# Performance work log

Measured on AMD Instinct MI355X. Metric: run time of the kernel, lower is better.

The kernel has to match this reference:

```python
import jax, jax.numpy as jnp
import numpy as np

HEADS = 12
DIM_HEAD = 64
SCALE = DIM_HEAD ** -0.5


def rotate_every_two(x):
    # (..., 2d) -> rotate pairs: (x1, x2) -> (-x2, x1)
    x = x.reshape(*x.shape[:-1], -1, 2)
    x1, x2 = x[..., 0], x[..., 1]
    return jnp.stack((-x2, x1), axis=-1).reshape(*x.shape[:-2], -1)


def apply_rotary_pos_emb(q, k, sinu_pos):
    # sinu_pos: (b, p, 2c) -> sin, cos each (b, p, c)
    b, p, two_c = sinu_pos.shape
    sp = sinu_pos.reshape(b, p, 2, two_c // 2)
    sin, cos = sp[:, :, 0, :], sp[:, :, 1, :]
    # interleave-repeat to (b, 1, p, 2c) to broadcast over heads
    sin = jnp.repeat(sin, 2, axis=-1)[:, None, :, :]
    cos = jnp.repeat(cos, 2, axis=-1)[:, None, :, :]
    rot = lambda t: t * cos + rotate_every_two(t) * sin
    return rot(q), rot(k)


def setup_inputs() -> dict:
    key = jax.random.key(0)
    ks = jax.random.split(key, 5)
    b, n, dim = 8, 1024, 768
    inner = HEADS * DIM_HEAD
    x = jax.random.normal(ks[0], (b, n, dim), dtype=jnp.float32)
    pos_emb = jax.random.normal(ks[1], (1, n, DIM_HEAD), dtype=jnp.float32)
    W_qkv = jax.random.normal(ks[2], (dim, 3 * inner), dtype=jnp.float32) * (dim ** -0.5)
    W_out = jax.random.normal(ks[3], (inner, dim), dtype=jnp.float32) * (inner ** -0.5)
    b_out = jnp.zeros((dim,), dtype=jnp.float32)
    return {"x": x, "pos_emb": pos_emb, "W_qkv": W_qkv, "W_out": W_out, "b_out": b_out}


def reference(x, pos_emb, W_qkv, W_out, b_out):
    b, n, _ = x.shape
    qkv = x @ W_qkv                                   # (b, n, 3*inner)
    q, k, v = jnp.split(qkv, 3, axis=-1)
    split_heads = lambda t: t.reshape(b, n, HEADS, DIM_HEAD).transpose(0, 2, 1, 3)
    q, k, v = split_heads(q), split_heads(k), split_heads(v)   # (b, h, n, d)
    q, k = apply_rotary_pos_emb(q, k, pos_emb)
    dots = jnp.einsum('bhid,bhjd->bhij', q, k) * SCALE
    attn = jax.nn.softmax(dots, axis=-1)
    out = jnp.einsum('bhij,bhjd->bhid', attn, v)
    out = out.transpose(0, 2, 1, 3).reshape(b, n, HEADS * DIM_HEAD)
    out = out @ W_out + b_out
    return out  # context is None -> torch code returns (out[:, :n], None); n == full length
```

## Files before the change

kernel.cpp:

```cpp
#include <hip/hip_runtime.h>
#include <hip/hip_bf16.h>

typedef __attribute__((ext_vector_type(8))) short bf16x8;
typedef __attribute__((ext_vector_type(4))) float f32x4;
typedef __attribute__((ext_vector_type(4))) unsigned short u16x4;
typedef unsigned short u16;
typedef unsigned int u32;

#define DEVINL __device__ __forceinline__

DEVINL u16 f2bf(float f) {
    union { float f; u32 u; } v; v.f = f;
    u32 r = v.u + 0x7FFFu + ((v.u >> 16) & 1u);
    return (u16)(r >> 16);
}
DEVINL float bf2f(u16 h) {
    union { u32 u; float f; } v; v.u = ((u32)h) << 16;
    return v.f;
}
DEVINL u32 cvt_pk_bf16(float lo, float hi) {
    u32 r;
    asm("v_cvt_pk_bf16_f32 %0, %1, %2" : "=v"(r) : "v"(lo), "v"(hi));
    return r;
}

template<int Nv> DEVINL void vmcnt_asm() {
    if constexpr (Nv == 0) asm volatile("s_waitcnt vmcnt(0)" ::: "memory");
    else if constexpr (Nv == 3) asm volatile("s_waitcnt vmcnt(3)" ::: "memory");
    else if constexpr (Nv == 5) asm volatile("s_waitcnt vmcnt(5)" ::: "memory");
    else if constexpr (Nv == 6) asm volatile("s_waitcnt vmcnt(6)" ::: "memory");
    else if constexpr (Nv == 7) asm volatile("s_waitcnt vmcnt(7)" ::: "memory");
    else asm volatile("s_waitcnt vmcnt(4)" ::: "memory");
}

#define GLOAD_LDS16(g, l) __builtin_amdgcn_global_load_lds( \
    (const __attribute__((address_space(1))) void*)(g), \
    (__attribute__((address_space(3))) void*)(l), 16, 0, 0)

#define SBAR() do { \
    __builtin_amdgcn_sched_barrier(0); \
    __builtin_amdgcn_s_barrier(); \
    __builtin_amdgcn_sched_barrier(0); } while (0)

__global__ __launch_bounds__(256) void prep_kernel(const float* __restrict__ x,
                                                   u16* __restrict__ xb,
                                                   const float* __restrict__ W_qkv,
                                                   u16* __restrict__ Wqkv_t,
                                                   const float* __restrict__ W_out,
                                                   u16* __restrict__ Wout_t) {
    __shared__ float tile[32][33];
    const int bid = blockIdx.x;
    if (bid < 3072) {
        int t = bid * 256 + threadIdx.x;
        const float4 v0 = reinterpret_cast<const float4*>(x)[t * 2];
        const float4 v1 = reinterpret_cast<const float4*>(x)[t * 2 + 1];
        u16 o[8];
        o[0] = f2bf(v0.x); o[1] = f2bf(v0.y); o[2] = f2bf(v0.z); o[3] = f2bf(v0.w);
        o[4] = f2bf(v1.x); o[5] = f2bf(v1.y); o[6] = f2bf(v1.z); o[7] = f2bf(v1.w);
        *reinterpret_cast<bf16x8*>(xb + (size_t)t * 8) = *reinterpret_cast<bf16x8*>(o);
        return;
    }
    const float* in; u16* out; int R, C, bx, by;
    if (bid < 4800) {
        int u = bid - 3072; in = W_qkv; out = Wqkv_t; R = 768; C = 2304;
        bx = u % 72; by = u / 72;
    } else {
        int u = bid - 4800; in = W_out; out = Wout_t; R = 768; C = 768;
        bx = u % 24; by = u / 24;
    }
    int c0 = bx * 32, r0 = by * 32;
    int tx = threadIdx.x & 31, ty = threadIdx.x >> 5;
#pragma unroll
    for (int i = 0; i < 4; ++i)
        tile[ty + i * 8][tx] = in[(size_t)(r0 + ty + i * 8) * C + c0 + tx];
    __syncthreads();
#pragma unroll
    for (int i = 0; i < 4; ++i)
        out[(size_t)(c0 + ty + i * 8) * R + r0 + tx] = f2bf(tile[tx][ty + i * 8]);
}

template<int K>
__global__ __launch_bounds__(256, 3) void gemm1_kernel(const u16* __restrict__ A,
                                                       const u16* __restrict__ Bt,
                                                       u16* __restrict__ Cout) {
    constexpr int NT = K / 32;
    constexpr int PBUF = (128 + 192) * 32;
    __shared__ u16 lds[2 * PBUF];

    const int tid = threadIdx.x;
    const int wv = tid >> 6, lane = tid & 63;
    const int lr = lane & 15, lg = lane >> 4;
    const int wr = wv >> 1, wc = wv & 1;

    const int id = blockIdx.x;
    const int sid = (id & 7) * 96 + (id >> 3);
    const int bm = (sid / 12) * 128;
    const int bn = (sid % 12) * 192;

#define STAGE(nb_, kt_) do { \
    _Pragma("unroll") \
    for (int j_ = 0; j_ < 2; ++j_) { \
        const int idx_ = j_ * 256 + tid; \
        const int row_ = idx_ >> 2; \
        const int c_ = (idx_ & 3) ^ ((row_ >> 1) & 3); \
        GLOAD_LDS16(A + (size_t)(bm + row_) * K + (kt_) * 32 + c_ * 8, \
                    (char*)lds + (nb_) * (PBUF * 2) + j_ * 4096 + tid * 16); \
    } \
    _Pragma("unroll") \
    for (int j_ = 0; j_ < 3; ++j_) { \
        const int idx_ = j_ * 256 + tid; \
        const int row_ = idx_ >> 2; \
        const int c_ = (idx_ & 3) ^ ((row_ >> 1) & 3); \
        GLOAD_LDS16(Bt + (size_t)(bn + row_) * K + (kt_) * 32 + c_ * 8, \
                    (char*)lds + (nb_) * (PBUF * 2) + 8192 + j_ * 4096 + tid * 16); \
    } } while (0)

    f32x4 acc[4][6];
#pragma unroll
    for (int i = 0; i < 4; ++i)
#pragma unroll
        for (int j = 0; j < 6; ++j) acc[i][j] = (f32x4){0.f, 0.f, 0.f, 0.f};

    STAGE(0, 0);
    __builtin_amdgcn_sched_barrier(0);
    vmcnt_asm<0>();
    SBAR();

    for (int kt = 0; kt < NT; ++kt) {
        const int cur = kt & 1;
        if (kt < NT - 1) {
            STAGE(cur ^ 1, kt + 1);
            __builtin_amdgcn_sched_barrier(0);
            vmcnt_asm<5>();
            SBAR();
        } else {
            __builtin_amdgcn_sched_barrier(0);
            vmcnt_asm<0>();
            SBAR();
        }
        bf16x8 af[4], bfr[6];
#pragma unroll
        for (int mf = 0; mf < 4; ++mf) {
            const int row = wr * 64 + mf * 16 + lr;
            af[mf] = *reinterpret_cast<const bf16x8*>(
                &lds[cur * PBUF + row * 32 + ((lg ^ ((row >> 1) & 3)) << 3)]);
        }
#pragma unroll
        for (int nf = 0; nf < 6; ++nf) {
            const int row = wc * 96 + nf * 16 + lr;
            bfr[nf] = *reinterpret_cast<const bf16x8*>(
                &lds[cur * PBUF + 4096 + row * 32 + ((lg ^ ((row >> 1) & 3)) << 3)]);
        }
        __builtin_amdgcn_s_setprio(1);
#pragma unroll
        for (int mf = 0; mf < 4; ++mf)
#pragma unroll
            for (int nf = 0; nf < 6; ++nf)
                acc[mf][nf] = __builtin_amdgcn_mfma_f32_16x16x32_bf16(
                    af[mf], bfr[nf], acc[mf][nf], 0, 0, 0);
        __builtin_amdgcn_s_setprio(0);
        SBAR();
    }

#pragma unroll
    for (int mf = 0; mf < 4; ++mf)
#pragma unroll
        for (int nf = 0; nf < 6; ++nf) {
            const int col = bn + wc * 96 + nf * 16 + lr;
#pragma unroll
            for (int r = 0; r < 4; ++r) {
                const int row = bm + wr * 64 + mf * 16 + lg * 4 + r;
                Cout[(size_t)row * 2304 + col] = f2bf(acc[mf][nf][r]);
            }
        }
#undef STAGE
}

template<int NTN, int NFRAG, int BROWS, int K, bool BF16_OUT>
__global__ __launch_bounds__(512, 2) void gemm_bigtile_kernel(const u16* __restrict__ A,
                                                              const u16* __restrict__ Bt,
                                                              void* __restrict__ Cout,
                                                              const float* __restrict__ bias) {
    constexpr int BN = NFRAG * 32;
    constexpr int N = NTN * BN;
    constexpr int NT = K / 64;
    constexpr int PA = 256 * 32;
    constexpr int PB = BROWS * 32;
    constexpr int PKS = PA + PB;
    constexpr int PBUF = 2 * PKS;
    constexpr int BFULL = (BROWS * 4) / 512;
    constexpr int BREM = (BROWS * 4) % 512;
    __shared__ u16 lds[2 * PBUF];

    const int tid = threadIdx.x;
    const int wv = tid >> 6, lane = tid & 63;
    const int lr = lane & 15, lg = lane >> 4;
    const int wr = wv >> 1, wc = wv & 1;

    const int id = blockIdx.x;
    const int sid = (id & 7) * 32 + (id >> 3);
    const int bm = (sid / NTN) * 256;
    const int bn = (sid % NTN) * BN;

#define PL(buf_, ks_, mat_) ((buf_) * PBUF + (ks_) * PKS + (mat_) * PA)

#define STAGE_A(nb_, kt_, ks_) do { \
    _Pragma("unroll") \
    for (int j_ = 0; j_ < 2; ++j_) { \
        const int idx_ = j_ * 512 + tid; \
        const int row_ = idx_ >> 2; \
        const int c_ = (idx_ & 3) ^ ((row_ >> 1) & 3); \
        GLOAD_LDS16(A + (size_t)(bm + row_) * K + (kt_) * 64 + (ks_) * 32 + c_ * 8, \
                    (char*)lds + PL((nb_), (ks_), 0) * 2 + j_ * 8192 + tid * 16); \
    } } while (0)

#define STAGE_B(nb_, kt_, ks_) do { \
    _Pragma("unroll") \
    for (int j_ = 0; j_ < BFULL; ++j_) { \
        const int idx_ = j_ * 512 + tid; \
        const int row_ = idx_ >> 2; \
        const int c_ = (idx_ & 3) ^ ((row_ >> 1) & 3); \
        GLOAD_LDS16(Bt + (size_t)(bn + row_) * K + (kt_) * 64 + (ks_) * 32 + c_ * 8, \
                    (char*)lds + PL((nb_), (ks_), 1) * 2 + j_ * 8192 + tid * 16); \
    } \
    if constexpr (BREM != 0) { \
        if (tid < BREM) { \
            const int idx_ = BFULL * 512 + tid; \
            const int row_ = idx_ >> 2; \
            const int c_ = (idx_ & 3) ^ ((row_ >> 1) & 3); \
            GLOAD_LDS16(Bt + (size_t)(bn + row_) * K + (kt_) * 64 + (ks_) * 32 + c_ * 8, \
                        (char*)lds + PL((nb_), (ks_), 1) * 2 + BFULL * 8192 + tid * 16); \
        } \
    } } while (0)

#define LDA(mh_, ks_, cur_) do { \
    _Pragma("unroll") \
    for (int f_ = 0; f_ < 2; ++f_) { \
        const int row_ = wr * 64 + (mh_) * 32 + f_ * 16 + lr; \
        af[f_] = *reinterpret_cast<const bf16x8*>( \
            &lds[PL((cur_), (ks_), 0) + row_ * 32 + ((lg ^ ((row_ >> 1) & 3)) << 3)]); \
    } } while (0)

#define LDB(ks_, cur_) do { \
    _Pragma("unroll") \
    for (int nf_ = 0; nf_ < NFRAG; ++nf_) { \
        const int row_ = wc * (NFRAG * 16) + nf_ * 16 + lr; \
        bfr[nf_] = *reinterpret_cast<const bf16x8*>( \
            &lds[PL((cur_), (ks_), 1) + row_ * 32 + ((lg ^ ((row_ >> 1) & 3)) << 3)]); \
    } } while (0)

#define MFMAQ(mh_) do { \
    __builtin_amdgcn_s_setprio(1); \
    _Pragma("unroll") \
    for (int f_ = 0; f_ < 2; ++f_) \
    _Pragma("unroll") \
    for (int nf_ = 0; nf_ < NFRAG; ++nf_) \
        acc[(mh_) * 2 + f_][nf_] = __builtin_amdgcn_mfma_f32_16x16x32_bf16( \
            af[f_], bfr[nf_], acc[(mh_) * 2 + f_][nf_], 0, 0, 0); \
    __builtin_amdgcn_s_setprio(0); } while (0)

#define WAITHALF() do { \
    __builtin_amdgcn_sched_barrier(0); \
    if constexpr (BREM != 0) { \
        if (wv < BREM / 64) vmcnt_asm<2 + BFULL + 1>(); \
        else vmcnt_asm<2 + BFULL>(); \
    } else { \
        vmcnt_asm<2 + BFULL>(); \
    } } while (0)

    f32x4 acc[4][NFRAG];
#pragma unroll
    for (int i = 0; i < 4; ++i)
#pragma unroll
        for (int j = 0; j < NFRAG; ++j) acc[i][j] = (f32x4){0.f, 0.f, 0.f, 0.f};

    bf16x8 af[2], bfr[NFRAG];

    STAGE_A(0, 0, 0); STAGE_B(0, 0, 0); STAGE_A(0, 0, 1); STAGE_B(0, 0, 1);
    __builtin_amdgcn_sched_barrier(0);
    vmcnt_asm<0>();
    SBAR();

    for (int kt = 0; kt < NT - 1; ++kt) {
        const int cur = kt & 1, nxt = cur ^ 1;
        LDB(0, cur); LDA(0, 0, cur);
        STAGE_A(nxt, kt + 1, 0);
        SBAR(); MFMAQ(0); SBAR();
        LDA(1, 0, cur);
        STAGE_B(nxt, kt + 1, 0);
        WAITHALF();
        SBAR(); MFMAQ(1); SBAR();
        LDB(1, cur); LDA(0, 1, cur);
        STAGE_A(nxt, kt + 1, 1);
        SBAR(); MFMAQ(0); SBAR();
        LDA(1, 1, cur);
        STAGE_B(nxt, kt + 1, 1);
        WAITHALF();
        SBAR(); MFMAQ(1); SBAR();
    }
    {
        const int cur = (NT - 1) & 1;
        LDB(0, cur); LDA(0, 0, cur); SBAR(); MFMAQ(0); SBAR();
        LDA(1, 0, cur);
        __builtin_amdgcn_sched_barrier(0);
        vmcnt_asm<0>();
        SBAR(); MFMAQ(1); SBAR();
        LDB(1, cur); LDA(0, 1, cur); SBAR(); MFMAQ(0); SBAR();
        LDA(1, 1, cur); SBAR(); MFMAQ(1);
    }

#pragma unroll
    for (int mf = 0; mf < 4; ++mf)
#pragma unroll
        for (int nf = 0; nf < NFRAG; ++nf) {
            const int col = bn + wc * (NFRAG * 16) + nf * 16 + lr;
            const float bv = BF16_OUT ? 0.f : bias[col];
#pragma unroll
            for (int r = 0; r < 4; ++r) {
                const int row = bm + wr * 64 + mf * 16 + lg * 4 + r;
                if (BF16_OUT)
                    ((u16*)Cout)[(size_t)row * N + col] = f2bf(acc[mf][nf][r]);
                else
                    ((float*)Cout)[(size_t)row * N + col] = acc[mf][nf][r] + bv;
            }
        }
#undef PL
#undef STAGE_A
#undef STAGE_B
#undef LDA
#undef LDB
#undef MFMAQ
#undef WAITHALF
}

__global__ __launch_bounds__(256) void rot_vtrans_kernel(u16* __restrict__ qkv,
                                                         const float* __restrict__ pos,
                                                         u16* __restrict__ Vt) {
    __shared__ u16 tile[64][72];
    const int bid = blockIdx.x;
    if (bid < 6144) {
        int t = bid * 256 + threadIdx.x;
        int row = t / 192;
        int col = (t % 192) * 8;
        int n = row & 1023;
        int i0 = (col & 63) >> 1;
        const float qs = (col < 768) ? 0.18033688f : 1.0f;
        const float* pn = pos + (size_t)n * 64;
        u16* p = qkv + (size_t)row * 2304 + col;
        bf16x8 v = *reinterpret_cast<bf16x8*>(p);
        u16 o[8];
#pragma unroll
        for (int j = 0; j < 4; ++j) {
            float s = pn[i0 + j], c = pn[32 + i0 + j];
            float x0 = bf2f((u16)v[2 * j]), x1 = bf2f((u16)v[2 * j + 1]);
            o[2 * j]     = f2bf((x0 * c - x1 * s) * qs);
            o[2 * j + 1] = f2bf((x1 * c + x0 * s) * qs);
        }
        *reinterpret_cast<bf16x8*>(p) = *reinterpret_cast<bf16x8*>(o);
    } else {
        int u = bid - 6144;
        int nt = u & 15;
        int bh = u >> 4;
        int b = bh / 12, h = bh % 12;
        int tid = threadIdx.x;
        int rr = tid >> 3, cc = (tid & 7) * 8;
#pragma unroll
        for (int it = 0; it < 2; ++it) {
            int nloc = it * 32 + rr;
            const u16* src = qkv + (size_t)(b * 1024 + nt * 64 + nloc) * 2304 + 1536 + h * 64 + cc;
            bf16x8 v = *reinterpret_cast<const bf16x8*>(src);
#pragma unroll
            for (int j = 0; j < 8; ++j) tile[nloc][cc + j] = (u16)v[j];
        }
        __syncthreads();
#pragma unroll
        for (int it = 0; it < 2; ++it) {
            int d = it * 32 + rr;
            u16 o[8];
#pragma unroll
            for (int j = 0; j < 8; ++j) o[j] = tile[cc + j][d];
            *reinterpret_cast<bf16x8*>(Vt + (size_t)(bh * 64 + d) * 1024 + nt * 64 + cc) =
                *reinterpret_cast<bf16x8*>(o);
        }
    }
}

__global__ __launch_bounds__(256, 3) void attn_kernel(const u16* __restrict__ qkv,
                                                      const u16* __restrict__ Vt,
                                                      u16* __restrict__ attn_out) {
    __shared__ u16 Ks[2][64 * 64];
    __shared__ u16 Vs[2][64 * 64];
    const int d_ = blockIdx.x;
    const int bh = ((d_ >> 3) >> 3) * 8 + (d_ & 7);
    const int qt = (d_ >> 3) & 7;
    const int b = bh / 12, h = bh % 12;
    const int tid = threadIdx.x;
    const int w = tid >> 6, lr = tid & 15, lg = (tid >> 4) & 3;

    bf16x8 qf[2][2];
#pragma unroll
    for (int q = 0; q < 2; ++q)
#pragma unroll
        for (int ds = 0; ds < 2; ++ds)
            qf[q][ds] = *reinterpret_cast<const bf16x8*>(
                &qkv[(size_t)(b * 1024 + qt * 128 + w * 32 + q * 16 + lr) * 2304 +
                     h * 64 + ds * 32 + lg * 8]);

    f32x4 o[2][4];
#pragma unroll
    for (int q = 0; q < 2; ++q)
#pragma unroll
        for (int i = 0; i < 4; ++i) o[q][i] = (f32x4){0.f, 0.f, 0.f, 0.f};
    float lsum[2] = {0.f, 0.f};

#define STAGE_KV(nb, kt_) do { \
    _Pragma("unroll") \
    for (int j_ = 0; j_ < 2; ++j_) { \
        const int idx_ = j_ * 256 + tid; \
        const int row_ = idx_ >> 3; \
        const int sc_ = ((idx_ & 7) ^ (row_ & 7)) * 8; \
        const int rk_ = (row_ & 0x20) | ((row_ & 0x0C) << 1) | ((row_ & 0x10) >> 2) | (row_ & 3); \
        GLOAD_LDS16(qkv + (size_t)(b * 1024 + (kt_) * 64 + rk_) * 2304 + 768 + h * 64 + sc_, \
                    (char*)Ks[nb] + idx_ * 16); \
        GLOAD_LDS16(Vt + (size_t)(bh * 64 + row_) * 1024 + (kt_) * 64 + sc_, \
                    (char*)Vs[nb] + idx_ * 16); \
    } } while (0)

    STAGE_KV(0, 0);
    __syncthreads();

    const int rsw = lr & 7;

    for (int kt = 0; kt < 16; ++kt) {
        const int cur = kt & 1;
        if (kt < 15) STAGE_KV(cur ^ 1, kt + 1);

        f32x4 s[2][4];
        __builtin_amdgcn_s_setprio(1);
#pragma unroll
        for (int kf = 0; kf < 4; ++kf) {
            bf16x8 k0 = *reinterpret_cast<const bf16x8*>(
                &Ks[cur][(kf * 16 + lr) * 64 + ((lg ^ rsw) * 8)]);
            bf16x8 k1 = *reinterpret_cast<const bf16x8*>(
                &Ks[cur][(kf * 16 + lr) * 64 + (((4 + lg) ^ rsw) * 8)]);
#pragma unroll
            for (int q = 0; q < 2; ++q) {
                f32x4 a = __builtin_amdgcn_mfma_f32_16x16x32_bf16(
                    k0, qf[q][0], (f32x4){0.f, 0.f, 0.f, 0.f}, 0, 0, 0);
                s[q][kf] = __builtin_amdgcn_mfma_f32_16x16x32_bf16(k1, qf[q][1], a, 0, 0, 0);
            }
        }
        __builtin_amdgcn_s_setprio(0);

        union { u32 wd[4]; bf16x8 v; } pk[2][2];
#pragma unroll
        for (int q = 0; q < 2; ++q) {
#pragma unroll
            for (int kf = 0; kf < 4; ++kf)
#pragma unroll
                for (int r = 0; r < 4; ++r) s[q][kf][r] = __builtin_amdgcn_exp2f(s[q][kf][r]);
            float t0 = (s[q][0][0] + s[q][0][1]) + (s[q][0][2] + s[q][0][3]);
            float t1 = (s[q][1][0] + s[q][1][1]) + (s[q][1][2] + s[q][1][3]);
            float t2 = (s[q][2][0] + s[q][2][1]) + (s[q][2][2] + s[q][2][3]);
            float t3 = (s[q][3][0] + s[q][3][1]) + (s[q][3][2] + s[q][3][3]);
            lsum[q] += (t0 + t1) + (t2 + t3);
#pragma unroll
            for (int ks = 0; ks < 2; ++ks) {
                pk[q][ks].wd[0] = cvt_pk_bf16(s[q][2 * ks][0], s[q][2 * ks][1]);
                pk[q][ks].wd[1] = cvt_pk_bf16(s[q][2 * ks][2], s[q][2 * ks][3]);
                pk[q][ks].wd[2] = cvt_pk_bf16(s[q][2 * ks + 1][0], s[q][2 * ks + 1][1]);
                pk[q][ks].wd[3] = cvt_pk_bf16(s[q][2 * ks + 1][2], s[q][2 * ks + 1][3]);
            }
        }

        __builtin_amdgcn_s_setprio(1);
#pragma unroll
        for (int ks = 0; ks < 2; ++ks) {
#pragma unroll
            for (int df = 0; df < 4; ++df) {
                bf16x8 vb = *reinterpret_cast<const bf16x8*>(
                    &Vs[cur][(df * 16 + lr) * 64 + (((ks * 4 + lg) ^ rsw) * 8)]);
                o[0][df] = __builtin_amdgcn_mfma_f32_16x16x32_bf16(vb, pk[0][ks].v, o[0][df], 0, 0, 0);
                o[1][df] = __builtin_amdgcn_mfma_f32_16x16x32_bf16(vb, pk[1][ks].v, o[1][df], 0, 0, 0);
            }
        }
        __builtin_amdgcn_s_setprio(0);
        __syncthreads();
    }
#undef STAGE_KV

#pragma unroll
    for (int q = 0; q < 2; ++q) {
        float l = lsum[q];
        l += __shfl_xor(l, 16);
        l += __shfl_xor(l, 32);
        const float linv = 1.0f / l;
        u16* orow = attn_out +
            (size_t)(b * 1024 + qt * 128 + w * 32 + q * 16 + lr) * 768 + h * 64 + lg * 4;
#pragma unroll
        for (int df = 0; df < 4; ++df) {
            uint2 st;
            st.x = cvt_pk_bf16(o[q][df][0] * linv, o[q][df][1] * linv);
            st.y = cvt_pk_bf16(o[q][df][2] * linv, o[q][df][3] * linv);
            *reinterpret_cast<uint2*>(orow + df * 16) = st;
        }
    }
}

extern "C" void kernel_launch(void* const* d_in, const int* in_sizes, int n_in,
                              void* d_out, int out_size, void* d_ws, size_t ws_size,
                              hipStream_t stream) {
    (void)in_sizes; (void)n_in; (void)out_size; (void)ws_size;
    const float* x     = (const float*)d_in[0];
    const float* pos   = (const float*)d_in[1];
    const float* W_qkv = (const float*)d_in[2];
    const float* W_out = (const float*)d_in[3];
    const float* b_out = (const float*)d_in[4];
    float* out = (float*)d_out;

    char* ws = (char*)d_ws;
    u16* xb     = (u16*)(ws);
    u16* Wqkv_t = (u16*)(ws + 12582912);
    u16* Wout_t = (u16*)(ws + 16171008);
    u16* qkv    = (u16*)(ws + 17399808);
    u16* Vt     = (u16*)(ws + 55148544);
    u16* attn_o = (u16*)(ws + 67731456);

    prep_kernel<<<5376, 256, 0, stream>>>(x, xb, W_qkv, Wqkv_t, W_out, Wout_t);
    gemm1_kernel<768><<<768, 256, 0, stream>>>(xb, Wqkv_t, qkv);
    rot_vtrans_kernel<<<7680, 256, 0, stream>>>(qkv, pos, Vt);
    attn_kernel<<<768, 256, 0, stream>>>(qkv, Vt, attn_o);
    gemm_bigtile_kernel<8, 3, 128, 768, false><<<256, 512, 0, stream>>>(attn_o, Wout_t, out, b_out);
}
```

Before: 109.2 us.

## Triple-buffer QKV GEMM and attention loads, widen GEMM N tile to 288

```diff
diff --git a/kernel.cpp b/kernel.cpp
--- a/kernel.cpp
+++ b/kernel.cpp
@@ -26,11 +26,16 @@
 
 template<int Nv> DEVINL void vmcnt_asm() {
     if constexpr (Nv == 0) asm volatile("s_waitcnt vmcnt(0)" ::: "memory");
+    else if constexpr (Nv == 2) asm volatile("s_waitcnt vmcnt(2)" ::: "memory");
     else if constexpr (Nv == 3) asm volatile("s_waitcnt vmcnt(3)" ::: "memory");
+    else if constexpr (Nv == 4) asm volatile("s_waitcnt vmcnt(4)" ::: "memory");
     else if constexpr (Nv == 5) asm volatile("s_waitcnt vmcnt(5)" ::: "memory");
     else if constexpr (Nv == 6) asm volatile("s_waitcnt vmcnt(6)" ::: "memory");
     else if constexpr (Nv == 7) asm volatile("s_waitcnt vmcnt(7)" ::: "memory");
-    else asm volatile("s_waitcnt vmcnt(4)" ::: "memory");
+    else if constexpr (Nv == 8) asm volatile("s_waitcnt vmcnt(8)" ::: "memory");
+    else if constexpr (Nv == 12) asm volatile("s_waitcnt vmcnt(12)" ::: "memory");
+    else if constexpr (Nv == 14) asm volatile("s_waitcnt vmcnt(14)" ::: "memory");
+    else asm volatile("s_waitcnt vmcnt(10)" ::: "memory");
 }
 
 #define GLOAD_LDS16(g, l) __builtin_amdgcn_global_load_lds( \
@@ -80,12 +85,12 @@
 }
 
 template<int K>
-__global__ __launch_bounds__(256, 3) void gemm1_kernel(const u16* __restrict__ A,
+__global__ __launch_bounds__(256, 2) void gemm1_kernel(const u16* __restrict__ A,
                                                        const u16* __restrict__ Bt,
                                                        u16* __restrict__ Cout) {
     constexpr int NT = K / 32;
-    constexpr int PBUF = (128 + 192) * 32;
-    __shared__ u16 lds[2 * PBUF];
+    constexpr int PBUF = (128 + 288) * 32;
+    __shared__ u16 lds[3 * PBUF];
 
     const int tid = threadIdx.x;
     const int wv = tid >> 6, lane = tid & 63;
@@ -93,9 +98,9 @@
     const int wr = wv >> 1, wc = wv & 1;
 
     const int id = blockIdx.x;
-    const int sid = (id & 7) * 96 + (id >> 3);
-    const int bm = (sid / 12) * 128;
-    const int bn = (sid % 12) * 192;
+    const int sid = (id & 7) * 64 + (id >> 3);
+    const int bm = (sid >> 3) * 128;
+    const int bn = (sid & 7) * 288;
 
 #define STAGE(nb_, kt_) do { \
     _Pragma("unroll") \
@@ -104,41 +109,50 @@
         const int row_ = idx_ >> 2; \
         const int c_ = (idx_ & 3) ^ ((row_ >> 1) & 3); \
         GLOAD_LDS16(A + (size_t)(bm + row_) * K + (kt_) * 32 + c_ * 8, \
-                    (char*)lds + (nb_) * (PBUF * 2) + j_ * 4096 + tid * 16); \
+                    (char*)lds + (nb_) * (PBUF * 2) + idx_ * 16); \
     } \
     _Pragma("unroll") \
-    for (int j_ = 0; j_ < 3; ++j_) { \
+    for (int j_ = 0; j_ < 4; ++j_) { \
         const int idx_ = j_ * 256 + tid; \
         const int row_ = idx_ >> 2; \
         const int c_ = (idx_ & 3) ^ ((row_ >> 1) & 3); \
         GLOAD_LDS16(Bt + (size_t)(bn + row_) * K + (kt_) * 32 + c_ * 8, \
-                    (char*)lds + (nb_) * (PBUF * 2) + 8192 + j_ * 4096 + tid * 16); \
-    } } while (0)
-
-    f32x4 acc[4][6];
+                    (char*)lds + (nb_) * (PBUF * 2) + 8192 + idx_ * 16); \
+    } \
+    if (tid < 128) { \
+        const int idx_ = 1024 + tid; \
+        const int row_ = idx_ >> 2; \
+        const int c_ = (idx_ & 3) ^ ((row_ >> 1) & 3); \
+        GLOAD_LDS16(Bt + (size_t)(bn + row_) * K + (kt_) * 32 + c_ * 8, \
+                    (char*)lds + (nb_) * (PBUF * 2) + 8192 + idx_ * 16); \
+    } } while (0)
+
+    f32x4 acc[4][9];
 #pragma unroll
     for (int i = 0; i < 4; ++i)
 #pragma unroll
-        for (int j = 0; j < 6; ++j) acc[i][j] = (f32x4){0.f, 0.f, 0.f, 0.f};
+        for (int j = 0; j < 9; ++j) acc[i][j] = (f32x4){0.f, 0.f, 0.f, 0.f};
 
     STAGE(0, 0);
-    __builtin_amdgcn_sched_barrier(0);
-    vmcnt_asm<0>();
-    SBAR();
+    STAGE(1, 1);
 
     for (int kt = 0; kt < NT; ++kt) {
-        const int cur = kt & 1;
-        if (kt < NT - 1) {
-            STAGE(cur ^ 1, kt + 1);
+        const int cur = kt % 3;
+        if (kt < NT - 2) {
+            STAGE((kt + 2) % 3, kt + 2);
             __builtin_amdgcn_sched_barrier(0);
-            vmcnt_asm<5>();
-            SBAR();
+            if (wv < 2) vmcnt_asm<14>();
+            else vmcnt_asm<12>();
+        } else if (kt == NT - 2) {
+            __builtin_amdgcn_sched_barrier(0);
+            if (wv < 2) vmcnt_asm<7>();
+            else vmcnt_asm<6>();
         } else {
             __builtin_amdgcn_sched_barrier(0);
             vmcnt_asm<0>();
-            SBAR();
-        }
-        bf16x8 af[4], bfr[6];
+        }
+        SBAR();
+        bf16x8 af[4], bfr[9];
 #pragma unroll
         for (int mf = 0; mf < 4; ++mf) {
             const int row = wr * 64 + mf * 16 + lr;
@@ -146,8 +160,8 @@
                 &lds[cur * PBUF + row * 32 + ((lg ^ ((row >> 1) & 3)) << 3)]);
         }
 #pragma unroll
-        for (int nf = 0; nf < 6; ++nf) {
-            const int row = wc * 96 + nf * 16 + lr;
+        for (int nf = 0; nf < 9; ++nf) {
+            const int row = wc * 144 + nf * 16 + lr;
             bfr[nf] = *reinterpret_cast<const bf16x8*>(
                 &lds[cur * PBUF + 4096 + row * 32 + ((lg ^ ((row >> 1) & 3)) << 3)]);
         }
@@ -155,7 +169,7 @@
 #pragma unroll
         for (int mf = 0; mf < 4; ++mf)
 #pragma unroll
-            for (int nf = 0; nf < 6; ++nf)
+            for (int nf = 0; nf < 9; ++nf)
                 acc[mf][nf] = __builtin_amdgcn_mfma_f32_16x16x32_bf16(
                     af[mf], bfr[nf], acc[mf][nf], 0, 0, 0);
         __builtin_amdgcn_s_setprio(0);
@@ -165,8 +179,8 @@
 #pragma unroll
     for (int mf = 0; mf < 4; ++mf)
 #pragma unroll
-        for (int nf = 0; nf < 6; ++nf) {
-            const int col = bn + wc * 96 + nf * 16 + lr;
+        for (int nf = 0; nf < 9; ++nf) {
+            const int col = bn + wc * 144 + nf * 16 + lr;
 #pragma unroll
             for (int r = 0; r < 4; ++r) {
                 const int row = bm + wr * 64 + mf * 16 + lg * 4 + r;
@@ -388,8 +402,8 @@
 __global__ __launch_bounds__(256, 3) void attn_kernel(const u16* __restrict__ qkv,
                                                       const u16* __restrict__ Vt,
                                                       u16* __restrict__ attn_out) {
-    __shared__ u16 Ks[2][64 * 64];
-    __shared__ u16 Vs[2][64 * 64];
+    __shared__ u16 Ks[3][64 * 64];
+    __shared__ u16 Vs[3][64 * 64];
     const int d_ = blockIdx.x;
     const int bh = ((d_ >> 3) >> 3) * 8 + (d_ & 7);
     const int qt = (d_ >> 3) & 7;
@@ -427,13 +441,24 @@
     } } while (0)
 
     STAGE_KV(0, 0);
-    __syncthreads();
+    STAGE_KV(1, 1);
 
     const int rsw = lr & 7;
 
     for (int kt = 0; kt < 16; ++kt) {
-        const int cur = kt & 1;
-        if (kt < 15) STAGE_KV(cur ^ 1, kt + 1);
+        const int cur = kt % 3;
+        if (kt < 14) {
+            STAGE_KV((kt + 2) % 3, kt + 2);
+            __builtin_amdgcn_sched_barrier(0);
+            vmcnt_asm<8>();
+        } else if (kt == 14) {
+            __builtin_amdgcn_sched_barrier(0);
+            vmcnt_asm<4>();
+        } else {
+            __builtin_amdgcn_sched_barrier(0);
+            vmcnt_asm<0>();
+        }
+        SBAR();
 
         f32x4 s[2][4];
         __builtin_amdgcn_s_setprio(1);
@@ -485,7 +510,7 @@
             }
         }
         __builtin_amdgcn_s_setprio(0);
-        __syncthreads();
+        SBAR();
     }
 #undef STAGE_KV
 
@@ -527,7 +552,7 @@
     u16* attn_o = (u16*)(ws + 67731456);
 
     prep_kernel<<<5376, 256, 0, stream>>>(x, xb, W_qkv, Wqkv_t, W_out, Wout_t);
-    gemm1_kernel<768><<<768, 256, 0, stream>>>(xb, Wqkv_t, qkv);
+    gemm1_kernel<768><<<512, 256, 0, stream>>>(xb, Wqkv_t, qkv);
     rot_vtrans_kernel<<<7680, 256, 0, stream>>>(qkv, pos, Vt);
     attn_kernel<<<768, 256, 0, stream>>>(qkv, Vt, attn_o);
     gemm_bigtile_kernel<8, 3, 128, 768, false><<<256, 512, 0, stream>>>(attn_o, Wout_t, out, b_out);
```

New measurement: 109.1 us. No clear change (-0.0%).
